# Kernel tuning notes

Measured on AMD Instinct MI355X. Metric: run time of the kernel, lower is better.

## Reference

```python
import jax, jax.numpy as jnp
import numpy as np

E = 1024
H = 16
HD = E // H  # 64
R = 8
ALPHA = 32
SCALING = ALPHA / R  # LoRA scaling = 4.0


def _lora_linear(x, W, b, A, B):
    # x: [..., in], W: [out, in], A: [r, in], B: [out, r]
    base = jnp.einsum('...i,oi->...o', x, W) + b
    lora = jnp.einsum('...r,or->...o', jnp.einsum('...i,ri->...r', x, A), B) * SCALING
    return base + lora


def setup_inputs() -> dict:
    key = jax.random.key(0)
    ks = jax.random.split(key, 20)
    L, N = 2048, 2
    d = {}
    d['query'] = jax.random.normal(ks[0], (L, N, E), dtype=jnp.float32)
    d['key_padding_mask'] = jax.random.randint(ks[1], (N, L), 0, 2) > 0
    i = 2
    for p in ('q', 'k', 'v', 'o'):
        d['W' + p] = jax.random.normal(ks[i], (E, E), dtype=jnp.float32) * (E ** -0.5); i += 1
        d['b' + p] = jax.random.normal(ks[i], (E,), dtype=jnp.float32) * 0.01; i += 1
        d['A' + p] = jax.random.normal(ks[i], (R, E), dtype=jnp.float32) * (E ** -0.5); i += 1
        d['B' + p] = jax.random.normal(ks[i], (E, R), dtype=jnp.float32) * 0.01; i += 1
    return d


def reference(query, key_padding_mask, Wq, bq, Aq, Bq, Wk, bk, Ak, Bk,
              Wv, bv, Av, Bv, Wo, bo, Ao, Bo):
    L, N, _ = query.shape
    q = _lora_linear(query, Wq, bq, Aq, Bq)  # [L, N, E]
    k = _lora_linear(query, Wk, bk, Ak, Bk)
    v = _lora_linear(query, Wv, bv, Av, Bv)

    def split_heads(x):  # [L, N, E] -> [N, H, L, HD]
        return x.transpose(1, 0, 2).reshape(N, L, H, HD).transpose(0, 2, 1, 3)

    scale = HD ** -0.5
    qh = split_heads(q) * scale
    kh = split_heads(k)
    vh = split_heads(v)

    logits = jnp.einsum('nhqd,nhkd->nhqk', qh, kh)  # [N, H, L, L]
    dt = logits.dtype
    pad = key_padding_mask[:, None, None, :]  # [N, 1, 1, Lk]
    logits = jnp.where(pad, jnp.finfo(dt).min, logits)
    logits = logits - jnp.max(logits, axis=-1, keepdims=True)
    w = jax.nn.softmax(logits, axis=-1)
    # zero out padded keys then renormalize (faithful to the module)
    w = jnp.where(pad, jnp.zeros((), dt), w)
    denom = jnp.maximum(jnp.sum(w, axis=-1, keepdims=True), jnp.finfo(dt).tiny)
    w = w / denom

    out = jnp.einsum('nhqk,nhkd->nhqd', w, vh)  # [N, H, L, HD]
    out = out.transpose(0, 2, 1, 3).reshape(N, L, E).transpose(1, 0, 2)  # [L, N, E]
    attn_output = _lora_linear(out, Wo, bo, Ao, Bo)

    # average_attn_weights=True path: mean over heads, then permute(1,0,2)
    attn_weights_out = jnp.mean(w, axis=1).transpose(1, 0, 2)  # [Lq, N, Lk]
    return attn_output, attn_weights_out
```

## Files before the change

### kernel.cpp

```cpp
#include <hip/hip_runtime.h>
#include <stdint.h>


typedef __attribute__((ext_vector_type(8))) short short8;
typedef __attribute__((ext_vector_type(4))) float f32x4;

#define LORA_SCALING 4.0f
#define FTINY 1.1754943508222875e-38f

static __device__ __forceinline__ unsigned short f2bf(float f){
  unsigned u = __float_as_uint(f);
  u += 0x7fffu + ((u >> 16) & 1u);
  return (unsigned short)(u >> 16);
}
static __device__ __forceinline__ float bflo(unsigned u){ return __uint_as_float(u << 16); }
static __device__ __forceinline__ float bfhi(unsigned u){ return __uint_as_float(u & 0xffff0000u); }
static __device__ __forceinline__ unsigned pk2(float lo, float hi){
  return (unsigned)f2bf(lo) | ((unsigned)f2bf(hi) << 16);
}
static __device__ __forceinline__ unsigned cvtpk(float lo, float hi){
  unsigned r;
  asm("v_cvt_pk_bf16_f32 %0, %1, %2" : "=v"(r) : "v"(lo), "v"(hi));
  return r;
}

union S8U { short8 v; uint2 u[2]; };

__global__ __launch_bounds__(256) void pack_bf16(const float* __restrict__ src,
                                                 unsigned short* __restrict__ dst)
{
  const size_t i = (size_t)blockIdx.x * 256 + threadIdx.x;
  const float4 f0 = ((const float4*)src)[i*2];
  const float4 f1 = ((const float4*)src)[i*2 + 1];
  ((uint4*)dst)[i] = make_uint4(pk2(f0.x,f0.y), pk2(f0.z,f0.w),
                                pk2(f1.x,f1.y), pk2(f1.z,f1.w));
}

__global__ __launch_bounds__(256) void xa_kernel(const unsigned short* __restrict__ X,
                                                 const float* __restrict__ A,
                                                 float* __restrict__ xa)
{
  __shared__ float red[4][8];
  const int t = blockIdx.x, tid = threadIdx.x;
  const int lane = tid & 63, wid = tid >> 6;

  const uint2 xr = *(const uint2*)(X + (size_t)t*1024 + tid*4);
  const float x0 = bflo(xr.x), x1 = bfhi(xr.x), x2 = bflo(xr.y), x3 = bfhi(xr.y);

  float acc[8];
#pragma unroll
  for (int r = 0; r < 8; ++r) {
    const float4 ar = *(const float4*)(A + (size_t)r*1024 + tid*4);
    acc[r] = x0*ar.x + x1*ar.y + x2*ar.z + x3*ar.w;
  }
#pragma unroll
  for (int r = 0; r < 8; ++r) {
    float v = acc[r];
#pragma unroll
    for (int off = 32; off > 0; off >>= 1) v += __shfl_xor(v, off, 64);
    if (lane == 0) red[wid][r] = v;
  }
  __syncthreads();
  if (tid < 8) xa[(size_t)t*8 + tid] = red[0][tid] + red[1][tid] + red[2][tid] + red[3][tid];
}

__global__ __launch_bounds__(256) void gemm_bf16(
    const unsigned short* __restrict__ Abf,
    const unsigned short* __restrict__ W0bf, const unsigned short* __restrict__ W1bf,
    const unsigned short* __restrict__ W2bf,
    const float* __restrict__ B0, const float* __restrict__ B1, const float* __restrict__ B2,
    const float* __restrict__ xa0, const float* __restrict__ xa1, const float* __restrict__ xa2,
    const float* __restrict__ L0, const float* __restrict__ L1, const float* __restrict__ L2,
    void* __restrict__ C0, void* __restrict__ C1, void* __restrict__ C2,
    int fp32out)
{
  const int z = blockIdx.z;
  const unsigned short* W = (z==0)?W0bf:((z==1)?W1bf:W2bf);
  const float* Bb = (z==0)?B0:((z==1)?B1:B2);
  const float* xa = (z==0)?xa0:((z==1)?xa1:xa2);
  const float* Lb = (z==0)?L0:((z==1)?L1:L2);
  void*        C  = (z==0)?C0:((z==1)?C1:C2);
  const bool vtw = (z == 2);

  __shared__ alignas(16) unsigned short As[128*32];
  __shared__ alignas(16) unsigned short Bs[128*32];

  const int tid = threadIdx.x;
  const int lane = tid & 63, wid = tid >> 6;
  const int quad = lane >> 4, lm = lane & 15;
  const int t0 = blockIdx.x * 128, n0 = blockIdx.y * 128;
  const int wm = (wid & 1) * 64, wn = (wid >> 1) * 64;

  const int srow = tid >> 1;
  const int shalf = (tid & 1) * 16;

  f32x4 acc[4][4];
#pragma unroll
  for (int i = 0; i < 4; ++i)
#pragma unroll
    for (int j = 0; j < 4; ++j) acc[i][j] = 0.f;

  for (int kt = 0; kt < 32; ++kt) {
    const int k0 = kt * 32;
    const unsigned short* ga = Abf + (size_t)(t0 + srow)*1024 + k0 + shalf;
    const uint4 a0 = *(const uint4*)ga;
    const uint4 a1 = *(const uint4*)(ga + 8);
    const unsigned short* gb = W + (size_t)(n0 + srow)*1024 + k0 + shalf;
    const uint4 b0 = *(const uint4*)gb;
    const uint4 b1 = *(const uint4*)(gb + 8);
    __syncthreads();
    *(uint4*)&As[srow*32 + shalf]     = a0;
    *(uint4*)&As[srow*32 + shalf + 8] = a1;
    *(uint4*)&Bs[srow*32 + shalf]     = b0;
    *(uint4*)&Bs[srow*32 + shalf + 8] = b1;
    __syncthreads();
    short8 a[4], b[4];
#pragma unroll
    for (int i = 0; i < 4; ++i) a[i] = *(const short8*)&As[(wm + i*16 + lm)*32 + quad*8];
#pragma unroll
    for (int j = 0; j < 4; ++j) b[j] = *(const short8*)&Bs[(wn + j*16 + lm)*32 + quad*8];
#pragma unroll
    for (int i = 0; i < 4; ++i)
#pragma unroll
      for (int j = 0; j < 4; ++j)
        acc[i][j] = __builtin_amdgcn_mfma_f32_16x16x32_bf16(a[i], b[j], acc[i][j], 0, 0, 0);
  }

#pragma unroll
  for (int j = 0; j < 4; ++j) {
    const int col = n0 + wn + j*16 + lm;
    const float bias = Bb[col];
    const float4 u0 = ((const float4*)(Lb + (size_t)col*8))[0];
    const float4 u1 = ((const float4*)(Lb + (size_t)col*8))[1];
#pragma unroll
    for (int i = 0; i < 4; ++i) {
#pragma unroll
      for (int r = 0; r < 4; ++r) {
        const int row = t0 + wm + i*16 + quad*4 + r;
        const float* xr = xa + (size_t)row*8;
        const float lora = xr[0]*u0.x + xr[1]*u0.y + xr[2]*u0.z + xr[3]*u0.w
                         + xr[4]*u1.x + xr[5]*u1.y + xr[6]*u1.z + xr[7]*u1.w;
        const float val = acc[i][j][r] + bias + LORA_SCALING*lora;
        if (fp32out) {
          ((float*)C)[(size_t)row*1024 + col] = val;
        } else if (vtw) {
          ((unsigned short*)C)[((size_t)(row & 1) * 1024 + col) * 2048 + (row >> 1)] = f2bf(val);
        } else {
          ((unsigned short*)C)[(size_t)row*1024 + col] = f2bf(val);
        }
      }
    }
  }
}

__global__ __launch_bounds__(256, 4) void attn_pv(
    const unsigned short* __restrict__ qb, const unsigned short* __restrict__ kb,
    const unsigned short* __restrict__ vt, const int* __restrict__ mask,
    unsigned short* __restrict__ ctx, float* __restrict__ msl)
{
  __shared__ alignas(16) unsigned short Es[64*132];
  __shared__ unsigned char mlds[2048];
  __shared__ float lred[4][64];

  const int tid = threadIdx.x, lane = tid & 63, wid = tid >> 6;
  const int quad = lane >> 4, lm = lane & 15;
  const int q0 = blockIdx.x * 64, n = blockIdx.y, h = blockIdx.z;

  {
    const int4 m0 = *(const int4*)(mask + n*2048 + tid*8);
    const int4 m1 = *(const int4*)(mask + n*2048 + tid*8 + 4);
    mlds[tid*8+0] = (m0.x != 0); mlds[tid*8+1] = (m0.y != 0);
    mlds[tid*8+2] = (m0.z != 0); mlds[tid*8+3] = (m0.w != 0);
    mlds[tid*8+4] = (m1.x != 0); mlds[tid*8+5] = (m1.y != 0);
    mlds[tid*8+6] = (m1.z != 0); mlds[tid*8+7] = (m1.w != 0);
  }

  short8 bq[4][2];
#pragma unroll
  for (int q_t = 0; q_t < 4; ++q_t) {
    const unsigned short* qg = qb + ((size_t)(q0 + q_t*16 + lm)*2 + n)*1024 + h*64 + quad*8;
    bq[q_t][0] = *(const short8*)qg;
    bq[q_t][1] = *(const short8*)(qg + 32);
  }

  float lsum[4] = {0.f, 0.f, 0.f, 0.f};
  f32x4 oacc[4];
#pragma unroll
  for (int dt = 0; dt < 4; ++dt) oacc[dt] = 0.f;

  for (int jt = 0; jt < 16; ++jt) {
    const int j0 = jt * 128;
    __syncthreads();

    f32x4 sacc[2][4];
#pragma unroll
    for (int a = 0; a < 2; ++a)
#pragma unroll
      for (int b = 0; b < 4; ++b) sacc[a][b] = 0.f;
#pragma unroll
    for (int kt = 0; kt < 2; ++kt) {
      short8 ak[2];
#pragma unroll
      for (int j_t = 0; j_t < 2; ++j_t)
        ak[j_t] = *(const short8*)(kb + ((size_t)(j0 + wid*32 + j_t*16 + lm)*2 + n)*1024 + h*64 + kt*32 + quad*8);
#pragma unroll
      for (int j_t = 0; j_t < 2; ++j_t)
#pragma unroll
        for (int q_t = 0; q_t < 4; ++q_t)
          sacc[j_t][q_t] = __builtin_amdgcn_mfma_f32_16x16x32_bf16(ak[j_t], bq[q_t][kt], sacc[j_t][q_t], 0, 0, 0);
    }
#pragma unroll
    for (int j_t = 0; j_t < 2; ++j_t) {
      const int jrow = wid*32 + j_t*16 + quad*4;
      const uchar4 mk = *(const uchar4*)&mlds[j0 + jrow];
#pragma unroll
      for (int q_t = 0; q_t < 4; ++q_t) {
        const float e0 = mk.x ? 0.f : __expf(sacc[j_t][q_t][0]*0.125f);
        const float e1 = mk.y ? 0.f : __expf(sacc[j_t][q_t][1]*0.125f);
        const float e2 = mk.z ? 0.f : __expf(sacc[j_t][q_t][2]*0.125f);
        const float e3 = mk.w ? 0.f : __expf(sacc[j_t][q_t][3]*0.125f);
        lsum[q_t] += (e0 + e1) + (e2 + e3);
        const int qcol = q_t*16 + lm;
        *(uint2*)&Es[qcol*132 + jrow] = make_uint2(cvtpk(e0, e1), cvtpk(e2, e3));
      }
    }
    __syncthreads();
#pragma unroll
    for (int kk = 0; kk < 4; ++kk) {
      S8U ae;
      const int r0 = wid*16 + lm;
      ae.u[0] = *(const uint2*)&Es[r0*132 + kk*32 + quad*8];
      ae.u[1] = *(const uint2*)&Es[r0*132 + kk*32 + quad*8 + 4];
      const unsigned short* vbase = vt + (size_t)((n*16 + h)*64)*2048 + j0 + kk*32 + quad*8;
#pragma unroll
      for (int dt = 0; dt < 4; ++dt) {
        const short8 bv = *(const short8*)(vbase + (size_t)(dt*16 + lm)*2048);
        oacc[dt] = __builtin_amdgcn_mfma_f32_16x16x32_bf16(ae.v, bv, oacc[dt], 0, 0, 0);
      }
    }
  }

#pragma unroll
  for (int q_t = 0; q_t < 4; ++q_t) {
    float v = lsum[q_t];
    v += __shfl_xor(v, 16, 64);
    v += __shfl_xor(v, 32, 64);
    if (quad == 0) lred[wid][q_t*16 + lm] = v;
  }
  __syncthreads();
  if (tid < 64) {
    const float l = lred[0][tid] + lred[1][tid] + lred[2][tid] + lred[3][tid];
    const float rinv = 1.0f / fmaxf(l, FTINY);
    lred[0][tid] = rinv;
    msl[(size_t)(h*2 + n)*2048 + q0 + tid] = rinv;
  }
  __syncthreads();
  {
    const int rb = wid*16 + quad*4;
    const float4 rv4 = *(const float4*)&lred[0][rb];
    const float rva[4] = {rv4.x, rv4.y, rv4.z, rv4.w};
#pragma unroll
    for (int dt = 0; dt < 4; ++dt) {
#pragma unroll
      for (int r = 0; r < 4; ++r) {
        ctx[((size_t)(q0 + rb + r)*2 + n)*1024 + h*64 + dt*16 + lm] =
            f2bf(oacc[dt][r] * rva[r]);
      }
    }
  }
}

__global__ __launch_bounds__(256, 4) void wmean2(
    const unsigned short* __restrict__ qb, const unsigned short* __restrict__ kb,
    const int* __restrict__ mask, const float* __restrict__ msl,
    float* __restrict__ wout)
{
  const int tid = threadIdx.x, lane = tid & 63, wid = tid >> 6;
  const int quad = lane >> 4, lm = lane & 15;
  const int q0 = blockIdx.x * 64, j0 = blockIdx.y * 128, n = blockIdx.z;
  const int wq = wid >> 1, wj = wid & 1;

  unsigned fm = 0;
#pragma unroll
  for (int j_t = 0; j_t < 4; ++j_t)
    fm |= (mask[n*2048 + j0 + wj*64 + j_t*16 + lm] != 0 ? 1u : 0u) << j_t;

  f32x4 wacc[2][4];
#pragma unroll
  for (int i = 0; i < 2; ++i)
#pragma unroll
    for (int j = 0; j < 4; ++j) wacc[i][j] = 0.f;

  for (int h = 0; h < 16; ++h) {
    short8 aq[2][2];
#pragma unroll
    for (int i = 0; i < 2; ++i) {
      const unsigned short* qg = qb + ((size_t)(q0 + wq*32 + i*16 + lm)*2 + n)*1024 + h*64 + quad*8;
      aq[i][0] = *(const short8*)qg;
      aq[i][1] = *(const short8*)(qg + 32);
    }
    float4 rv[2];
#pragma unroll
    for (int i = 0; i < 2; ++i)
      rv[i] = *(const float4*)&msl[(size_t)(h*2 + n)*2048 + q0 + wq*32 + i*16 + quad*4];
#pragma unroll
    for (int jh2 = 0; jh2 < 2; ++jh2) {
      short8 bk[2][2];
#pragma unroll
      for (int jtl = 0; jtl < 2; ++jtl) {
        const unsigned short* kg = kb + ((size_t)(j0 + wj*64 + (jh2*2 + jtl)*16 + lm)*2 + n)*1024 + h*64 + quad*8;
        bk[jtl][0] = *(const short8*)kg;
        bk[jtl][1] = *(const short8*)(kg + 32);
      }
      f32x4 sacc[2][2];
#pragma unroll
      for (int i = 0; i < 2; ++i)
#pragma unroll
        for (int jtl = 0; jtl < 2; ++jtl) sacc[i][jtl] = 0.f;
#pragma unroll
      for (int kt = 0; kt < 2; ++kt)
#pragma unroll
        for (int i = 0; i < 2; ++i)
#pragma unroll
          for (int jtl = 0; jtl < 2; ++jtl)
            sacc[i][jtl] = __builtin_amdgcn_mfma_f32_16x16x32_bf16(aq[i][kt], bk[jtl][kt], sacc[i][jtl], 0, 0, 0);
#pragma unroll
      for (int i = 0; i < 2; ++i) {
        const float rva[4] = {rv[i].x, rv[i].y, rv[i].z, rv[i].w};
#pragma unroll
        for (int jtl = 0; jtl < 2; ++jtl) {
          const int j_t = jh2*2 + jtl;
          const bool mskd = (fm >> j_t) & 1u;
#pragma unroll
          for (int r = 0; r < 4; ++r) {
            const float e = mskd ? 0.f : __expf(sacc[i][jtl][r]*0.125f) * rva[r];
            wacc[i][j_t][r] += e;
          }
        }
      }
    }
  }
#pragma unroll
  for (int i = 0; i < 2; ++i)
#pragma unroll
    for (int j_t = 0; j_t < 4; ++j_t)
#pragma unroll
      for (int r = 0; r < 4; ++r) {
        const int row = q0 + wq*32 + i*16 + quad*4 + r;
        const int col = j0 + wj*64 + j_t*16 + lm;
        wout[((size_t)row*2 + n)*2048 + col] = wacc[i][j_t][r] * 0.0625f;
      }
}

__global__ __launch_bounds__(256) void ctx_copy(const uint4* __restrict__ src,
                                                uint4* __restrict__ dst)
{
  const size_t i = (size_t)blockIdx.x * 256 + threadIdx.x;
  dst[i] = src[i];
}

extern "C" void kernel_launch(void* const* d_in, const int* in_sizes, int n_in,
                              void* d_out, int out_size, void* d_ws, size_t ws_size,
                              hipStream_t stream) {
  const float* x    = (const float*)d_in[0];
  const int*   mask = (const int*)d_in[1];
  const float* Wq = (const float*)d_in[2];  const float* bq = (const float*)d_in[3];
  const float* Aq = (const float*)d_in[4];  const float* Bq = (const float*)d_in[5];
  const float* Wk = (const float*)d_in[6];  const float* bk = (const float*)d_in[7];
  const float* Ak = (const float*)d_in[8];  const float* Bk = (const float*)d_in[9];
  const float* Wv = (const float*)d_in[10]; const float* bv = (const float*)d_in[11];
  const float* Av = (const float*)d_in[12]; const float* Bv = (const float*)d_in[13];
  const float* Wo = (const float*)d_in[14]; const float* bo = (const float*)d_in[15];
  const float* Ao = (const float*)d_in[16]; const float* Bo = (const float*)d_in[17];

  float* outF = (float*)d_out;
  float* woutF = outF + 4194304;

  unsigned short* kbuf = (unsigned short*)d_ws;
  unsigned short* vtb  = kbuf + 4194304;
  unsigned short* qbuf = vtb  + 4194304;

  float* xaq = woutF;
  float* xak = xaq + 32768;
  float* xav = xak + 32768;

  unsigned short* Xbf  = (unsigned short*)outF;
  unsigned short* Wqbf = (unsigned short*)(outF + 2097152);
  unsigned short* Wkbf = (unsigned short*)(outF + 2621440);
  unsigned short* Wvbf = (unsigned short*)(outF + 3145728);
  unsigned short* ctx16 = (unsigned short*)outF;
  float* msl = outF + 2359296;

  float* xao = (float*)vtb;
  unsigned short* Wobf = vtb + 524288;

  pack_bf16<<<dim3(2048), dim3(256), 0, stream>>>(x, Xbf);
  pack_bf16<<<dim3(512),  dim3(256), 0, stream>>>(Wq, Wqbf);
  pack_bf16<<<dim3(512),  dim3(256), 0, stream>>>(Wk, Wkbf);
  pack_bf16<<<dim3(512),  dim3(256), 0, stream>>>(Wv, Wvbf);

  xa_kernel<<<dim3(4096), dim3(256), 0, stream>>>(Xbf, Aq, xaq);
  xa_kernel<<<dim3(4096), dim3(256), 0, stream>>>(Xbf, Ak, xak);
  xa_kernel<<<dim3(4096), dim3(256), 0, stream>>>(Xbf, Av, xav);

  gemm_bf16<<<dim3(32, 8, 3), dim3(256), 0, stream>>>(
      Xbf, Wqbf, Wkbf, Wvbf, bq, bk, bv, xaq, xak, xav, Bq, Bk, Bv,
      qbuf, kbuf, vtb, 0);

  attn_pv<<<dim3(32, 2, 16), dim3(256), 0, stream>>>(qbuf, kbuf, vtb, mask, ctx16, msl);

  pack_bf16<<<dim3(512), dim3(256), 0, stream>>>(Wo, Wobf);

  wmean2<<<dim3(32, 16, 2), dim3(256), 0, stream>>>(qbuf, kbuf, mask, msl, woutF);

  ctx_copy<<<dim3(2048), dim3(256), 0, stream>>>((const uint4*)ctx16, (uint4*)kbuf);

  xa_kernel<<<dim3(4096), dim3(256), 0, stream>>>(kbuf, Ao, xao);

  gemm_bf16<<<dim3(32, 8, 1), dim3(256), 0, stream>>>(
      kbuf, Wobf, Wobf, Wobf, bo, bo, bo, xao, xao, xao, Bo, Bo, Bo,
      outF, outF, outF, 1);
}
```

Measured before the change: 542.5 us.

## Use direct global-to-LDS loads in GEMM, fold softmax scale into Q projection

The projection GEMM now stages tiles with global_load_lds 16-byte direct loads instead of loading into registers and storing to LDS. The 1/sqrt(d) scale is applied in the Q GEMM epilogue, so the attention and weight-mean kernels no longer multiply before each exp. The occupancy hint of 4 blocks per CU is dropped from attn_pv and wmean2, which gives the compiler more registers per thread but may reduce resident waves. Folding the scale before bf16 rounding slightly changes numerics, but 0.125 is a power of two, so the effect is negligible.

```diff
diff --git a/kernel.cpp b/kernel.cpp
--- a/kernel.cpp
+++ b/kernel.cpp
@@ -22,6 +22,11 @@
   unsigned r;
   asm("v_cvt_pk_bf16_f32 %0, %1, %2" : "=v"(r) : "v"(lo), "v"(hi));
   return r;
+}
+static __device__ __forceinline__ void gload16(const void* g, void* l){
+  __builtin_amdgcn_global_load_lds(
+      (const __attribute__((address_space(1))) unsigned int*)g,
+      (__attribute__((address_space(3))) unsigned int*)l, 16, 0, 0);
 }
 
 union S8U { short8 v; uint2 u[2]; };
@@ -72,7 +77,7 @@
     const float* __restrict__ xa0, const float* __restrict__ xa1, const float* __restrict__ xa2,
     const float* __restrict__ L0, const float* __restrict__ L1, const float* __restrict__ L2,
     void* __restrict__ C0, void* __restrict__ C1, void* __restrict__ C2,
-    int fp32out)
+    int fp32out, float scale0)
 {
   const int z = blockIdx.z;
   const unsigned short* W = (z==0)?W0bf:((z==1)?W1bf:W2bf);
@@ -81,6 +86,7 @@
   const float* Lb = (z==0)?L0:((z==1)?L1:L2);
   void*        C  = (z==0)?C0:((z==1)?C1:C2);
   const bool vtw = (z == 2);
+  const float sc = (z == 0) ? scale0 : 1.0f;
 
   __shared__ alignas(16) unsigned short As[128*32];
   __shared__ alignas(16) unsigned short Bs[128*32];
@@ -91,8 +97,9 @@
   const int t0 = blockIdx.x * 128, n0 = blockIdx.y * 128;
   const int wm = (wid & 1) * 64, wn = (wid >> 1) * 64;
 
-  const int srow = tid >> 1;
-  const int shalf = (tid & 1) * 16;
+  const int c0 = tid, c1 = tid + 256;
+  const int r0c = c0 >> 2, e0c = (c0 & 3) * 8;
+  const int r1c = c1 >> 2, e1c = (c1 & 3) * 8;
 
   f32x4 acc[4][4];
 #pragma unroll
@@ -102,17 +109,11 @@
 
   for (int kt = 0; kt < 32; ++kt) {
     const int k0 = kt * 32;
-    const unsigned short* ga = Abf + (size_t)(t0 + srow)*1024 + k0 + shalf;
-    const uint4 a0 = *(const uint4*)ga;
-    const uint4 a1 = *(const uint4*)(ga + 8);
-    const unsigned short* gb = W + (size_t)(n0 + srow)*1024 + k0 + shalf;
-    const uint4 b0 = *(const uint4*)gb;
-    const uint4 b1 = *(const uint4*)(gb + 8);
     __syncthreads();
-    *(uint4*)&As[srow*32 + shalf]     = a0;
-    *(uint4*)&As[srow*32 + shalf + 8] = a1;
-    *(uint4*)&Bs[srow*32 + shalf]     = b0;
-    *(uint4*)&Bs[srow*32 + shalf + 8] = b1;
+    gload16(Abf + (size_t)(t0 + r0c)*1024 + k0 + e0c, &As[c0*8]);
+    gload16(Abf + (size_t)(t0 + r1c)*1024 + k0 + e1c, &As[c1*8]);
+    gload16(W   + (size_t)(n0 + r0c)*1024 + k0 + e0c, &Bs[c0*8]);
+    gload16(W   + (size_t)(n0 + r1c)*1024 + k0 + e1c, &Bs[c1*8]);
     __syncthreads();
     short8 a[4], b[4];
 #pragma unroll
@@ -140,7 +141,7 @@
         const float* xr = xa + (size_t)row*8;
         const float lora = xr[0]*u0.x + xr[1]*u0.y + xr[2]*u0.z + xr[3]*u0.w
                          + xr[4]*u1.x + xr[5]*u1.y + xr[6]*u1.z + xr[7]*u1.w;
-        const float val = acc[i][j][r] + bias + LORA_SCALING*lora;
+        const float val = (acc[i][j][r] + bias + LORA_SCALING*lora) * sc;
         if (fp32out) {
           ((float*)C)[(size_t)row*1024 + col] = val;
         } else if (vtw) {
@@ -153,7 +154,7 @@
   }
 }
 
-__global__ __launch_bounds__(256, 4) void attn_pv(
+__global__ __launch_bounds__(256) void attn_pv(
     const unsigned short* __restrict__ qb, const unsigned short* __restrict__ kb,
     const unsigned short* __restrict__ vt, const int* __restrict__ mask,
     unsigned short* __restrict__ ctx, float* __restrict__ msl)
@@ -215,10 +216,10 @@
       const uchar4 mk = *(const uchar4*)&mlds[j0 + jrow];
 #pragma unroll
       for (int q_t = 0; q_t < 4; ++q_t) {
-        const float e0 = mk.x ? 0.f : __expf(sacc[j_t][q_t][0]*0.125f);
-        const float e1 = mk.y ? 0.f : __expf(sacc[j_t][q_t][1]*0.125f);
-        const float e2 = mk.z ? 0.f : __expf(sacc[j_t][q_t][2]*0.125f);
-        const float e3 = mk.w ? 0.f : __expf(sacc[j_t][q_t][3]*0.125f);
+        const float e0 = mk.x ? 0.f : __expf(sacc[j_t][q_t][0]);
+        const float e1 = mk.y ? 0.f : __expf(sacc[j_t][q_t][1]);
+        const float e2 = mk.z ? 0.f : __expf(sacc[j_t][q_t][2]);
+        const float e3 = mk.w ? 0.f : __expf(sacc[j_t][q_t][3]);
         lsum[q_t] += (e0 + e1) + (e2 + e3);
         const int qcol = q_t*16 + lm;
         *(uint2*)&Es[qcol*132 + jrow] = make_uint2(cvtpk(e0, e1), cvtpk(e2, e3));
@@ -270,7 +271,7 @@
   }
 }
 
-__global__ __launch_bounds__(256, 4) void wmean2(
+__global__ __launch_bounds__(256) void wmean2(
     const unsigned short* __restrict__ qb, const unsigned short* __restrict__ kb,
     const int* __restrict__ mask, const float* __restrict__ msl,
     float* __restrict__ wout)
@@ -333,7 +334,7 @@
           const bool mskd = (fm >> j_t) & 1u;
 #pragma unroll
           for (int r = 0; r < 4; ++r) {
-            const float e = mskd ? 0.f : __expf(sacc[i][jtl][r]*0.125f) * rva[r];
+            const float e = mskd ? 0.f : __expf(sacc[i][jtl][r]) * rva[r];
             wacc[i][j_t][r] += e;
           }
         }
@@ -405,7 +406,7 @@
 
   gemm_bf16<<<dim3(32, 8, 3), dim3(256), 0, stream>>>(
       Xbf, Wqbf, Wkbf, Wvbf, bq, bk, bv, xaq, xak, xav, Bq, Bk, Bv,
-      qbuf, kbuf, vtb, 0);
+      qbuf, kbuf, vtb, 0, 0.125f);
 
   attn_pv<<<dim3(32, 2, 16), dim3(256), 0, stream>>>(qbuf, kbuf, vtb, mask, ctx16, msl);
 
@@ -419,5 +420,5 @@
 
   gemm_bf16<<<dim3(32, 8, 1), dim3(256), 0, stream>>>(
       kbuf, Wobf, Wobf, Wobf, bo, bo, bo, xao, xao, xao, Bo, Bo, Bo,
-      outF, outF, outF, 1);
-}
+      outF, outF, outF, 1, 1.0f);
+}
```

Result: slower. 589.4 us (+8.7%).
